# Kernel optimization log

Measured on AMD Instinct MI355X. Metric: run time of the kernel, lower is better.

## Reference

```python
import jax, jax.numpy as jnp
import numpy as np


def setup_inputs() -> dict:
    key = jax.random.key(0)
    ks = jax.random.split(key, 5)
    B, T, C, H, E = 8, 2048, 1024, 2048, 8
    n_layer = 12
    x = jax.random.normal(ks[0], (B, T, C), dtype=jnp.float32)
    w_router = jax.random.normal(ks[1], (C, E), dtype=jnp.float32) * 0.02
    w_c_fc = jax.random.normal(ks[2], (E, C, H), dtype=jnp.float32) * 0.02
    w_gate = jax.random.normal(ks[3], (E, C, H), dtype=jnp.float32) * 0.02
    w_c_proj = jax.random.normal(ks[4], (E, H, C), dtype=jnp.float32) * (0.02 * (2 * n_layer) ** -0.5)
    return {
        "x": x, "w_router": w_router, "w_c_fc": w_c_fc,
        "w_gate": w_gate, "w_c_proj": w_c_proj,
        "top_k": 2, "n_experts": E, "expert_capacity": 640,
    }


def reference(x, w_router, w_c_fc, w_gate, w_c_proj, top_k, n_experts, expert_capacity):
    B, T, C = x.shape
    # ---- router ----
    gate_logits = jnp.einsum('btc,ce->bte', x, w_router)
    gate_probs = jax.nn.softmax(gate_logits, axis=-1)  # (B,T,E)

    # ---- per-batch top-k dispatch (cumsum slot assignment + scatter) ----
    def dispatch(xb, pb):
        # xb: (T,C), pb: (T,E)
        topk_p, topk_i = jax.lax.top_k(pb, top_k)              # (T,k)
        ei = jnp.swapaxes(topk_i, 0, 1).ravel()                # (k*T,) k-major
        oh = jax.nn.one_hot(ei, n_experts, dtype=jnp.int32)    # (k*T,E)
        pos = jnp.cumsum(oh, axis=0) * oh - 1                  # slot within expert
        pos = jnp.swapaxes(pos.reshape(top_k, T, n_experts), 0, 1).max(axis=2)  # (T,k)
        ei = jnp.swapaxes(ei.reshape(top_k, T), 0, 1)          # (T,k)
        buf = jnp.zeros((n_experts, expert_capacity, C), dtype=xb.dtype)
        xr = jnp.repeat(xb, top_k, axis=0)                     # (T*k,C) token-major
        buf = buf.at[ei.ravel(), pos.ravel()].set(xr)          # overflow slots dropped
        return topk_p, pos, ei, buf

    topk_p, pos, ei, buf = jax.vmap(dispatch)(x, gate_probs)   # buf: (B,E,cap,C)

    # ---- batched expert SwiGLU GEMMs ----
    ein = jnp.swapaxes(buf, 0, 1).reshape(n_experts, B * expert_capacity, C)
    h = jnp.einsum('eti,eih->eth', ein, w_c_fc)
    g = jax.nn.silu(jnp.einsum('eti,eih->eth', ein, w_gate))
    o = jnp.einsum('eth,eho->eto', g * h, w_c_proj)
    eo = jnp.swapaxes(o.reshape(n_experts, B, expert_capacity, C), 0, 1)  # (B,E,cap,C)

    # ---- weighted combine gather ----
    def combine(eo_b, i_b, p_b, pr_b):
        sel = eo_b[i_b, p_b]                                   # (T,k,C)
        return jnp.sum(pr_b[..., None] * sel, axis=1)          # (T,C)

    y = jax.vmap(combine)(eo, ei, pos, topk_p)                 # (B,T,C)
    return y
```

## Files before the change

kernel.cpp:

```cpp
#include <hip/hip_runtime.h>
#include <stdint.h>

#define B_   8
#define T_   2048
#define C_   1024
#define H_   2048
#define E_   8
#define CAP_ 640
#define RPE_ (B_*CAP_)
#define BT_  (B_*T_)

typedef __attribute__((ext_vector_type(8))) short bf16x8;
typedef __attribute__((ext_vector_type(4))) float f32x4;

static __device__ __forceinline__ unsigned short f2bf(float f){
  union { float f; uint32_t u; } a; a.f = f;
  uint32_t u = a.u;
  uint32_t r = (u + 0x7FFFu + ((u >> 16) & 1u)) >> 16;
  return (unsigned short)r;
}

#define GLD16(gp, lp) __builtin_amdgcn_global_load_lds( \
    (__attribute__((address_space(1))) void*)(gp), \
    (__attribute__((address_space(3))) void*)(lp), 16, 0, 0)

#define VMW(N) asm volatile("s_waitcnt vmcnt(" #N ")" ::: "memory")
#define FENCE  asm volatile("" ::: "memory")
#define BARS   do { FENCE; __builtin_amdgcn_s_barrier(); __builtin_amdgcn_sched_barrier(0); } while(0)
#define BARE   do { __builtin_amdgcn_sched_barrier(0); FENCE; __builtin_amdgcn_s_barrier(); FENCE; } while(0)

#define LDA(H) do { \
  _Pragma("unroll") for (int ks_=0; ks_<2; ++ks_) \
  _Pragma("unroll") for (int f_=0; f_<4; ++f_) \
    pa[ks_][f_] = *(const bf16x8*)(bufc + (H)*16384u + aRow + (unsigned)f_*2048u + cc[ks_]); \
} while(0)
#define LDB(PB, H) do { \
  _Pragma("unroll") for (int ks_=0; ks_<2; ++ks_) \
  _Pragma("unroll") for (int n_=0; n_<2; ++n_) \
    PB[ks_][n_] = *(const bf16x8*)(bufc + 32768u + (H)*16384u + bRow + (unsigned)n_*2048u + cc[ks_]); \
} while(0)
#define MM16(Q, PB) do { \
  __builtin_amdgcn_s_setprio(1); \
  _Pragma("unroll") for (int ks_=0; ks_<2; ++ks_) \
  _Pragma("unroll") for (int f_=0; f_<4; ++f_) \
  _Pragma("unroll") for (int n_=0; n_<2; ++n_) \
    acc[Q][f_][n_] = __builtin_amdgcn_mfma_f32_16x16x32_bf16(pa[ks_][f_], PB[ks_][n_], acc[Q][f_][n_], 0,0,0); \
  __builtin_amdgcn_s_setprio(0); \
} while(0)

#define STG_A(H, T1) do { \
  unsigned kb_ = (unsigned)(T1)*128u; \
  unsigned db_ = ((unsigned)(T1)&1u)*65536u + (H)*16384u; \
  GLD16(pA##H##0 + kb_, lds + db_ + d0); \
  GLD16(pA##H##1 + kb_, lds + db_ + 8192u + d0); \
} while(0)
#define STG_B(H, T1) do { \
  unsigned kb_ = (unsigned)(T1)*128u; \
  unsigned db_ = ((unsigned)(T1)&1u)*65536u + 32768u + (H)*16384u; \
  GLD16(pB##H##0 + kb_, lds + db_ + d0); \
  GLD16(pB##H##1 + kb_, lds + db_ + 8192u + d0); \
} while(0)

__global__ __launch_bounds__(256) void router_kernel(
    const float* __restrict__ x, const float* __restrict__ wr,
    unsigned short* __restrict__ xbf, float* __restrict__ probs2, int* __restrict__ idx2)
{
  int bt = blockIdx.x;
  int tid = threadIdx.x;
  const float4 v = ((const float4*)(x + (size_t)bt*C_))[tid];
  ushort4 u;
  u.x = f2bf(v.x); u.y = f2bf(v.y); u.z = f2bf(v.z); u.w = f2bf(v.w);
  ((ushort4*)(xbf + (size_t)bt*C_))[tid] = u;

  double p[8];
  #pragma unroll
  for (int e=0;e<8;e++) p[e]=0.0;
  const float xv[4] = {v.x, v.y, v.z, v.w};
  #pragma unroll
  for (int j=0;j<4;j++){
    int c = tid*4+j;
    const float* wrow = wr + c*8;
    #pragma unroll
    for (int e=0;e<8;e++) p[e] += (double)xv[j] * (double)wrow[e];
  }
  __shared__ double red[8][256];
  #pragma unroll
  for (int e=0;e<8;e++) red[e][tid] = p[e];
  __syncthreads();
  for (int s=128; s>0; s>>=1){
    if (tid < s){
      #pragma unroll
      for (int e=0;e<8;e++) red[e][tid] += red[e][tid+s];
    }
    __syncthreads();
  }
  if (tid==0){
    double lg[8];
    #pragma unroll
    for (int e=0;e<8;e++) lg[e]=red[e][0];
    double mx = lg[0];
    #pragma unroll
    for (int e=1;e<8;e++) if (lg[e]>mx) mx=lg[e];
    double s=0.0, ex[8];
    #pragma unroll
    for (int e=0;e<8;e++){ ex[e]=exp(lg[e]-mx); s+=ex[e]; }
    int i1=0; double b1=ex[0];
    #pragma unroll
    for (int e=1;e<8;e++) if (ex[e]>b1){ b1=ex[e]; i1=e; }
    int i2=-1; double b2=-1.0;
    #pragma unroll
    for (int e=0;e<8;e++) if (e!=i1 && ex[e]>b2){ b2=ex[e]; i2=e; }
    probs2[bt*2+0] = (float)(b1/s);
    probs2[bt*2+1] = (float)(b2/s);
    idx2[bt*2+0] = i1;
    idx2[bt*2+1] = i2;
  }
}

__global__ __launch_bounds__(256) void transp_fcg_kernel(
    const float* __restrict__ fc, const float* __restrict__ gate,
    unsigned short* __restrict__ dst)
{
  __shared__ float t[32][33];
  int e = blockIdx.z;
  int n0 = blockIdx.x*32, k0 = blockIdx.y*32;
  int tx = threadIdx.x & 31, ty = threadIdx.x >> 5;
  #pragma unroll
  for (int sel=0; sel<2; ++sel){
    const float* s = (sel ? gate : fc) + ((size_t)e*C_ + k0)*H_ + n0;
    #pragma unroll
    for (int i=0;i<32;i+=8) t[ty+i][tx] = s[(size_t)(ty+i)*H_ + tx];
    __syncthreads();
    #pragma unroll
    for (int i=0;i<32;i+=8){
      int jj = ty+i;
      int drow = n0*2 + ((jj & 16) << 1) + sel*16 + (jj & 15);
      dst[((size_t)e*4096 + drow)*1024 + k0 + tx] = f2bf(t[tx][jj]);
    }
    __syncthreads();
  }
}

__global__ __launch_bounds__(256) void transp_kernel(
    const float* __restrict__ src, unsigned short* __restrict__ dst, int K, int N)
{
  __shared__ float t[32][33];
  int e = blockIdx.z;
  int n0 = blockIdx.x*32, k0 = blockIdx.y*32;
  int tx = threadIdx.x & 31, ty = threadIdx.x >> 5;
  const float* s = src + ((size_t)e*K + k0)*N + n0;
  #pragma unroll
  for (int i=0;i<32;i+=8) t[ty+i][tx] = s[(size_t)(ty+i)*N + tx];
  __syncthreads();
  unsigned short* d = dst + ((size_t)e*N + n0)*K + k0;
  #pragma unroll
  for (int i=0;i<32;i+=8) d[(size_t)(ty+i)*K + tx] = f2bf(t[tx][ty+i]);
}

__global__ void scan_kernel(const int* __restrict__ idx2, int* __restrict__ pos, int* __restrict__ cnt)
{
  int b = blockIdx.x, lane = threadIdx.x;
  unsigned long long below = (lane == 0) ? 0ull : (~0ull >> (64 - lane));
  int base = 0;
  for (int k=0;k<2;k++){
    for (int c0=0;c0<T_;c0+=64){
      int t = c0 + lane;
      int e = idx2[((b*T_ + t)<<1) + k];
      unsigned long long mym = 0; int addv = 0;
      #pragma unroll
      for (int ee=0; ee<8; ++ee){
        unsigned long long m = __ballot(e == ee);
        if (ee == e) mym = m;
        if (lane == ee) addv = __popcll(m);
      }
      int mybase = __shfl(base, e, 64);
      pos[((b*T_+t)<<1)+k] = mybase + __popcll(mym & below);
      base += addv;
    }
  }
  if (lane < 8) cnt[b*8 + lane] = (base < CAP_) ? base : CAP_;
}

__global__ void offsets_kernel(const int* __restrict__ cnt, int* __restrict__ off, int* __restrict__ Me)
{
  int e = threadIdx.x;
  if (e < 8){
    int s = 0;
    for (int b=0;b<8;b++){ off[e*8+b] = s; s += cnt[b*8+e]; }
    Me[e] = s;
  }
}

__global__ void fill_kernel(const int* __restrict__ idx2, const int* __restrict__ pos,
                            const int* __restrict__ off, const float* __restrict__ probs2,
                            int* __restrict__ token_src, float* __restrict__ row_prob)
{
  int a = blockIdx.x*256 + threadIdx.x;
  if (a >= BT_*2) return;
  int bt = a >> 1, k = a & 1;
  int b = bt >> 11;
  int e = idx2[bt*2+k];
  int p = pos[bt*2+k];
  if (p < CAP_){
    int r = e*RPE_ + off[e*8+b] + p;
    token_src[r] = bt;
    row_prob[r] = probs2[bt*2+k];
  }
}

__global__ __launch_bounds__(512, 2) void gemm1_kernel(
    const unsigned short* __restrict__ xbf,
    const unsigned short* __restrict__ wifcg,
    const int* __restrict__ token_src,
    const int* __restrict__ Me,
    unsigned short* __restrict__ act,
    int e0)
{
  const int lin = blockIdx.x;
  const int ez = lin / 320;
  const int r_ = lin % 320;
  const int xcd = r_ & 7, slot = r_ >> 3;
  const int nt = xcd + ((slot / 20) << 3);
  const int mt = slot % 20;
  const int e = e0 + ez;
  const int M = Me[e];
  if (mt*256 >= M) return;

  __shared__ __align__(16) unsigned char lds[131072];

  const int tid = threadIdx.x;
  const int w = tid >> 6, l = tid & 63;
  const int wm = w >> 2, wn = w & 3;
  const int l15 = l & 15, g0 = l >> 4;
  const unsigned d0 = (unsigned)tid * 16u;

  const int srow0 = tid >> 3, c0 = tid & 7;
  const unsigned scb = (unsigned)((c0 ^ (srow0 & 7)) * 16);
  const unsigned char* gA = (const unsigned char*)xbf;
  const unsigned char* gB = (const unsigned char*)wifcg;
  const int abase = e*RPE_ + mt*256;
  const unsigned char* pA00 = gA + (size_t)token_src[abase +       srow0]*2048u + scb;
  const unsigned char* pA01 = gA + (size_t)token_src[abase +  64 + srow0]*2048u + scb;
  const unsigned char* pA10 = gA + (size_t)token_src[abase + 128 + srow0]*2048u + scb;
  const unsigned char* pA11 = gA + (size_t)token_src[abase + 192 + srow0]*2048u + scb;
  const size_t bbase = (size_t)(ez*4096 + nt*256 + srow0);
  const unsigned char* pB00 = gB + (bbase +   0)*2048u + scb;
  const unsigned char* pB01 = gB + (bbase +  64)*2048u + scb;
  const unsigned char* pB10 = gB + (bbase + 128)*2048u + scb;
  const unsigned char* pB11 = gB + (bbase + 192)*2048u + scb;

  const unsigned aRow = (unsigned)((wm*64 + l15) * 128);
  const unsigned bRow = (unsigned)((wn*32 + l15) * 128);
  unsigned cc[2];
  cc[0] = (unsigned)(((0*4 + g0) ^ (l15 & 7)) * 16);
  cc[1] = (unsigned)(((1*4 + g0) ^ (l15 & 7)) * 16);

  f32x4 acc[4][4][2];
  #pragma unroll
  for (int p=0;p<4;++p)
    #pragma unroll
    for (int f=0;f<4;++f)
      #pragma unroll
      for (int n=0;n<2;++n) acc[p][f][n] = (f32x4){0.f,0.f,0.f,0.f};

  bf16x8 pa[2][4], pb0[2][2], pb1[2][2];

  STG_A(0,0); STG_B(0,0); STG_B(1,0); STG_A(1,0);
  VMW(4);
  FENCE; __builtin_amdgcn_s_barrier(); FENCE;

  const int NT = 16;
  for (int t = 0; t < NT-1; ++t){
    const unsigned char* bufc = lds + (unsigned)(t&1)*65536u;
    LDA(0); LDB(pb0,0); STG_A(0,t+1); VMW(4); BARS; MM16(0,pb0); BARE;
    LDB(pb1,1);         STG_B(0,t+1); VMW(4); BARS; MM16(1,pb1); BARE;
    LDA(1);             STG_B(1,t+1);         BARS; MM16(2,pb0); BARE;
                        STG_A(1,t+1); VMW(4); BARS; MM16(3,pb1); BARE;
  }
  {
    const unsigned char* bufc = lds + (unsigned)((NT-1)&1)*65536u;
    LDA(0); LDB(pb0,0); VMW(2); BARS; MM16(0,pb0); BARE;
    LDB(pb1,1);         VMW(0); BARS; MM16(1,pb1); BARE;
    LDA(1);                     BARS; MM16(2,pb0); BARE;
                                BARS; MM16(3,pb1); BARE;
  }

  const int r4 = (l >> 4) * 4;
  #pragma unroll
  for (int p=0;p<4;++p){
    const int ah = p>>1, bh = p&1;
    #pragma unroll
    for (int f=0;f<4;++f){
      const int grow = mt*256 + ah*128 + wm*64 + f*16 + r4;
      const int hcol = nt*128 + bh*64 + wn*16 + l15;
      #pragma unroll
      for (int r=0;r<4;++r){
        float h = acc[p][f][0][r];
        float gv = acc[p][f][1][r];
        float a = (gv / (1.f + __expf(-gv))) * h;
        act[((size_t)ez*RPE_ + grow + r)*(size_t)H_ + hcol] = f2bf(a);
      }
    }
  }
}

__global__ __launch_bounds__(512, 2) void gemm2_kernel(
    const unsigned short* __restrict__ act,
    const unsigned short* __restrict__ wprojT,
    const int* __restrict__ token_src,
    const float* __restrict__ row_prob,
    const int* __restrict__ Me,
    float* __restrict__ y,
    int e0)
{
  const int ez = blockIdx.z, e = e0 + ez, mt = blockIdx.y, nt = blockIdx.x;
  const int M = Me[e];
  if (mt*256 >= M) return;

  __shared__ __align__(16) unsigned char lds[131072];

  const int tid = threadIdx.x;
  const int w = tid >> 6, l = tid & 63;
  const int wm = w >> 2, wn = w & 3;
  const int l15 = l & 15, g0 = l >> 4;
  const unsigned d0 = (unsigned)tid * 16u;

  const int srow0 = tid >> 3, c0 = tid & 7;
  const unsigned scb = (unsigned)((c0 ^ (srow0 & 7)) * 16);
  const unsigned char* gA = (const unsigned char*)act;
  const unsigned char* gB = (const unsigned char*)wprojT;
  const size_t abase = (size_t)(ez*RPE_ + mt*256 + srow0);
  const unsigned char* pA00 = gA + (abase +   0)*4096u + scb;
  const unsigned char* pA01 = gA + (abase +  64)*4096u + scb;
  const unsigned char* pA10 = gA + (abase + 128)*4096u + scb;
  const unsigned char* pA11 = gA + (abase + 192)*4096u + scb;
  const size_t bbase = (size_t)(ez*C_ + nt*256 + srow0);
  const unsigned char* pB00 = gB + (bbase +   0)*4096u + scb;
  const unsigned char* pB01 = gB + (bbase +  64)*4096u + scb;
  const unsigned char* pB10 = gB + (bbase + 128)*4096u + scb;
  const unsigned char* pB11 = gB + (bbase + 192)*4096u + scb;

  const unsigned aRow = (unsigned)((wm*64 + l15) * 128);
  const unsigned bRow = (unsigned)((wn*32 + l15) * 128);
  unsigned cc[2];
  cc[0] = (unsigned)(((0*4 + g0) ^ (l15 & 7)) * 16);
  cc[1] = (unsigned)(((1*4 + g0) ^ (l15 & 7)) * 16);

  f32x4 acc[4][4][2];
  #pragma unroll
  for (int p=0;p<4;++p)
    #pragma unroll
    for (int f=0;f<4;++f)
      #pragma unroll
      for (int n=0;n<2;++n) acc[p][f][n] = (f32x4){0.f,0.f,0.f,0.f};

  bf16x8 pa[2][4], pb0[2][2], pb1[2][2];

  STG_A(0,0); STG_B(0,0); STG_B(1,0); STG_A(1,0);
  VMW(4);
  FENCE; __builtin_amdgcn_s_barrier(); FENCE;

  const int NT = 32;
  for (int t = 0; t < NT-1; ++t){
    const unsigned char* bufc = lds + (unsigned)(t&1)*65536u;
    LDA(0); LDB(pb0,0); STG_A(0,t+1); VMW(4); BARS; MM16(0,pb0); BARE;
    LDB(pb1,1);         STG_B(0,t+1); VMW(4); BARS; MM16(1,pb1); BARE;
    LDA(1);             STG_B(1,t+1);         BARS; MM16(2,pb0); BARE;
                        STG_A(1,t+1); VMW(4); BARS; MM16(3,pb1); BARE;
  }
  {
    const unsigned char* bufc = lds + (unsigned)((NT-1)&1)*65536u;
    LDA(0); LDB(pb0,0); VMW(2); BARS; MM16(0,pb0); BARE;
    LDB(pb1,1);         VMW(0); BARS; MM16(1,pb1); BARE;
    LDA(1);                     BARS; MM16(2,pb0); BARE;
                                BARS; MM16(3,pb1); BARE;
  }

  const int r4 = (l >> 4) * 4;
  #pragma unroll
  for (int p=0;p<4;++p){
    const int ah = p>>1, bh = p&1;
    #pragma unroll
    for (int f=0;f<4;++f){
      #pragma unroll
      for (int r=0;r<4;++r){
        const int rloc = mt*256 + ah*128 + wm*64 + f*16 + r4 + r;
        if (rloc < M){
          const int bt = token_src[e*RPE_ + rloc];
          const float pp = row_prob[e*RPE_ + rloc];
          float* yrow = y + (size_t)bt*C_;
          const int colb = nt*256 + bh*128 + wn*32 + l15;
          atomicAdd(yrow + colb,      pp * acc[p][f][0][r]);
          atomicAdd(yrow + colb + 16, pp * acc[p][f][1][r]);
        }
      }
    }
  }
}

extern "C" void kernel_launch(void* const* d_in, const int* in_sizes, int n_in,
                              void* d_out, int out_size, void* d_ws, size_t ws_size,
                              hipStream_t stream)
{
  const float* x   = (const float*)d_in[0];
  const float* wr  = (const float*)d_in[1];
  const float* wfc = (const float*)d_in[2];
  const float* wg  = (const float*)d_in[3];
  const float* wpj = (const float*)d_in[4];
  float* y = (float*)d_out;

  unsigned char* ws = (unsigned char*)d_ws;
  const size_t szXBF  = (size_t)BT_*C_*2;
  const size_t szFCGc = (size_t)2*4096*1024*2;
  const size_t szWPc  = (size_t)2*C_*H_*2;
  const size_t szFCGa = (size_t)E_*4096*1024*2;
  const size_t szWPa  = (size_t)E_*C_*H_*2;
  const size_t szMISC = 3*131072 + 2*(size_t)E_*RPE_*4 + 1024;

  const size_t need_small = szXBF + szFCGc + szWPc + (size_t)2*RPE_*H_*2 + szMISC;
  const size_t need_big2  = szXBF + szFCGa + szWPa  + (size_t)2*RPE_*H_*2 + szMISC;
  const size_t need_big4  = szXBF + szFCGa + szWPa  + (size_t)4*RPE_*H_*2 + szMISC;
  if (ws_size < need_small) return;
  const bool big4 = (ws_size >= need_big4);
  const bool big  = big4 || (ws_size >= need_big2);
  const int  ne   = big4 ? 4 : 2;

  const size_t szFCG = big ? szFCGa : szFCGc;
  const size_t szWP  = big ? szWPa  : szWPc;
  const size_t szACT = (size_t)ne*RPE_*H_*2;

  size_t oXBF = 0;
  size_t oFCG = oXBF + szXBF;
  size_t oWP  = oFCG + szFCG;
  size_t oACT = oWP  + szWP;
  size_t oM   = oACT + szACT;

  unsigned short* xbf    = (unsigned short*)(ws + oXBF);
  unsigned short* wifcg  = (unsigned short*)(ws + oFCG);
  unsigned short* wprojT = (unsigned short*)(ws + oWP);
  unsigned short* actc   = (unsigned short*)(ws + oACT);

  float* probs2    = (float*)(ws + oM);
  int*   idx2      = (int*)(ws + oM + 1*131072);
  int*   pos       = (int*)(ws + oM + 2*131072);
  int*   token_src = (int*)(ws + oM + 3*131072);
  float* row_prob  = (float*)(ws + oM + 3*131072 + (size_t)E_*RPE_*4);
  int*   cnt       = (int*)(ws + oM + 3*131072 + 2*(size_t)E_*RPE_*4);
  int*   off       = cnt + 64;
  int*   Me        = off + 64;

  hipMemsetAsync(y, 0, (size_t)out_size*4, stream);
  hipMemsetAsync(token_src, 0, (size_t)E_*RPE_*4, stream);

  router_kernel<<<BT_, 256, 0, stream>>>(x, wr, xbf, probs2, idx2);
  scan_kernel<<<B_, 64, 0, stream>>>(idx2, pos, cnt);
  offsets_kernel<<<1, 64, 0, stream>>>(cnt, off, Me);
  fill_kernel<<<(BT_*2+255)/256, 256, 0, stream>>>(idx2, pos, off, probs2, token_src, row_prob);

  if (big){
    transp_fcg_kernel<<<dim3(H_/32, C_/32, E_), 256, 0, stream>>>(wfc, wg, wifcg);
    transp_kernel<<<dim3(C_/32, H_/32, E_), 256, 0, stream>>>(wpj, wprojT, H_, C_);
  }

  for (int e0 = 0; e0 < E_; e0 += ne){
    unsigned short* wfcg_c = wifcg;
    unsigned short* wpj_c  = wprojT;
    if (big){
      wfcg_c = wifcg  + (size_t)e0*4096*1024;
      wpj_c  = wprojT + (size_t)e0*C_*H_;
    } else {
      transp_fcg_kernel<<<dim3(H_/32, C_/32, ne), 256, 0, stream>>>(
          wfc + (size_t)e0*C_*H_, wg + (size_t)e0*C_*H_, wifcg);
      transp_kernel<<<dim3(C_/32, H_/32, ne), 256, 0, stream>>>(
          wpj + (size_t)e0*H_*C_, wprojT, H_, C_);
    }
    gemm1_kernel<<<dim3(320*ne), 512, 0, stream>>>(
        xbf, wfcg_c, token_src, Me, actc, e0);
    gemm2_kernel<<<dim3(4, 20, ne), 512, 0, stream>>>(
        actc, wpj_c, token_src, row_prob, Me, y, e0);
  }
}
```

Measured before the change: 792.0 us.

## Rewrite gemm2 with 128x128 tiles, 256 threads, and XCD-aware block mapping

Replaces the 256x256-tile, 512-thread, hand-pipelined gemm2 with a simpler 128x128-tile kernel of 256 threads. It uses double-buffered 64 KB LDS and a flat 1D grid that maps blocks so neighbouring M tiles spread across XCDs. Smaller tiles raise occupancy and finer skipping of empty rows beyond Me. In exchange the kernel does more redundant global loads per FLOP and drops the interleaved fine-grained pipelining of the old schedule.

Result: faster. 741.3 us (-6.4%).

```diff
diff --git a/kernel.cpp b/kernel.cpp
--- a/kernel.cpp
+++ b/kernel.cpp
@@ -304,7 +304,7 @@
   }
 }
 
-__global__ __launch_bounds__(512, 2) void gemm2_kernel(
+__global__ __launch_bounds__(256) void gemm2_kernel(
     const unsigned short* __restrict__ act,
     const unsigned short* __restrict__ wprojT,
     const int* __restrict__ token_src,
@@ -313,85 +313,98 @@
     float* __restrict__ y,
     int e0)
 {
-  const int ez = blockIdx.z, e = e0 + ez, mt = blockIdx.y, nt = blockIdx.x;
+  const int lin = blockIdx.x;
+  const int ez = lin / 320;
+  const int r_ = lin % 320;
+  const int xcd = r_ & 7, slot = r_ >> 3;
+  const int mt = xcd + ((slot >> 3) << 3);
+  const int nt = slot & 7;
+  const int e = e0 + ez;
   const int M = Me[e];
-  if (mt*256 >= M) return;
-
-  __shared__ __align__(16) unsigned char lds[131072];
+  if (mt*128 >= M) return;
+
+  __shared__ __align__(16) unsigned char lds[2][32768];
 
   const int tid = threadIdx.x;
   const int w = tid >> 6, l = tid & 63;
-  const int wm = w >> 2, wn = w & 3;
-  const int l15 = l & 15, g0 = l >> 4;
-  const unsigned d0 = (unsigned)tid * 16u;
-
-  const int srow0 = tid >> 3, c0 = tid & 7;
-  const unsigned scb = (unsigned)((c0 ^ (srow0 & 7)) * 16);
+  const int wrow = w >> 1, wcol = w & 1;
+  const int r8 = l >> 3;
+  const unsigned swz16 = (unsigned)(((l & 7) ^ r8) * 16);
+
+  unsigned ldsOff[4];
+  size_t offA[4], offB[4];
+  #pragma unroll
+  for (int j = 0; j < 4; ++j){
+    int row = w*32 + j*8 + r8;
+    offA[j] = ((size_t)(ez*RPE_ + mt*128 + row))*4096u + swz16;
+    offB[j] = ((size_t)(ez*C_   + nt*128 + row))*4096u + swz16;
+    ldsOff[j] = (unsigned)(w*32 + j*8) * 128u;
+  }
+
+  f32x4 acc[4][4];
+  #pragma unroll
+  for (int i=0;i<4;i++)
+    #pragma unroll
+    for (int j=0;j<4;j++) acc[i][j] = (f32x4){0.f,0.f,0.f,0.f};
+
   const unsigned char* gA = (const unsigned char*)act;
   const unsigned char* gB = (const unsigned char*)wprojT;
-  const size_t abase = (size_t)(ez*RPE_ + mt*256 + srow0);
-  const unsigned char* pA00 = gA + (abase +   0)*4096u + scb;
-  const unsigned char* pA01 = gA + (abase +  64)*4096u + scb;
-  const unsigned char* pA10 = gA + (abase + 128)*4096u + scb;
-  const unsigned char* pA11 = gA + (abase + 192)*4096u + scb;
-  const size_t bbase = (size_t)(ez*C_ + nt*256 + srow0);
-  const unsigned char* pB00 = gB + (bbase +   0)*4096u + scb;
-  const unsigned char* pB01 = gB + (bbase +  64)*4096u + scb;
-  const unsigned char* pB10 = gB + (bbase + 128)*4096u + scb;
-  const unsigned char* pB11 = gB + (bbase + 192)*4096u + scb;
-
-  const unsigned aRow = (unsigned)((wm*64 + l15) * 128);
-  const unsigned bRow = (unsigned)((wn*32 + l15) * 128);
-  unsigned cc[2];
-  cc[0] = (unsigned)(((0*4 + g0) ^ (l15 & 7)) * 16);
-  cc[1] = (unsigned)(((1*4 + g0) ^ (l15 & 7)) * 16);
-
-  f32x4 acc[4][4][2];
-  #pragma unroll
-  for (int p=0;p<4;++p)
-    #pragma unroll
-    for (int f=0;f<4;++f)
-      #pragma unroll
-      for (int n=0;n<2;++n) acc[p][f][n] = (f32x4){0.f,0.f,0.f,0.f};
-
-  bf16x8 pa[2][4], pb0[2][2], pb1[2][2];
-
-  STG_A(0,0); STG_B(0,0); STG_B(1,0); STG_A(1,0);
-  VMW(4);
-  FENCE; __builtin_amdgcn_s_barrier(); FENCE;
-
+
+  auto stage = [&](int kt, int bb){
+    const unsigned kb = (unsigned)kt * 128u;
+    #pragma unroll
+    for (int j=0;j<4;++j) GLD16(gA + offA[j] + kb, &lds[bb][0]     + ldsOff[j]);
+    #pragma unroll
+    for (int j=0;j<4;++j) GLD16(gB + offB[j] + kb, &lds[bb][16384] + ldsOff[j]);
+  };
+  auto compute = [&](int bb){
+    #pragma unroll
+    for (int kh=0; kh<2; ++kh){
+      bf16x8 afr[4], bfr[4];
+      #pragma unroll
+      for (int fm=0; fm<4; ++fm){
+        int row = wrow*64 + fm*16 + (l & 15);
+        int gnum = kh*4 + (l >> 4);
+        int byt = row*128 + ((gnum ^ (row & 7)) * 16);
+        afr[fm] = *(const bf16x8*)(&lds[bb][0] + byt);
+      }
+      #pragma unroll
+      for (int fn=0; fn<4; ++fn){
+        int row = wcol*64 + fn*16 + (l & 15);
+        int gnum = kh*4 + (l >> 4);
+        int byt = row*128 + ((gnum ^ (row & 7)) * 16);
+        bfr[fn] = *(const bf16x8*)(&lds[bb][16384] + byt);
+      }
+      #pragma unroll
+      for (int fm=0; fm<4; ++fm)
+        #pragma unroll
+        for (int fn=0; fn<4; ++fn)
+          acc[fm][fn] = __builtin_amdgcn_mfma_f32_16x16x32_bf16(afr[fm], bfr[fn], acc[fm][fn], 0,0,0);
+    }
+  };
+
+  stage(0, 0);
+  __syncthreads();
   const int NT = 32;
-  for (int t = 0; t < NT-1; ++t){
-    const unsigned char* bufc = lds + (unsigned)(t&1)*65536u;
-    LDA(0); LDB(pb0,0); STG_A(0,t+1); VMW(4); BARS; MM16(0,pb0); BARE;
-    LDB(pb1,1);         STG_B(0,t+1); VMW(4); BARS; MM16(1,pb1); BARE;
-    LDA(1);             STG_B(1,t+1);         BARS; MM16(2,pb0); BARE;
-                        STG_A(1,t+1); VMW(4); BARS; MM16(3,pb1); BARE;
-  }
-  {
-    const unsigned char* bufc = lds + (unsigned)((NT-1)&1)*65536u;
-    LDA(0); LDB(pb0,0); VMW(2); BARS; MM16(0,pb0); BARE;
-    LDB(pb1,1);         VMW(0); BARS; MM16(1,pb1); BARE;
-    LDA(1);                     BARS; MM16(2,pb0); BARE;
-                                BARS; MM16(3,pb1); BARE;
-  }
-
-  const int r4 = (l >> 4) * 4;
-  #pragma unroll
-  for (int p=0;p<4;++p){
-    const int ah = p>>1, bh = p&1;
-    #pragma unroll
-    for (int f=0;f<4;++f){
-      #pragma unroll
-      for (int r=0;r<4;++r){
-        const int rloc = mt*256 + ah*128 + wm*64 + f*16 + r4 + r;
-        if (rloc < M){
-          const int bt = token_src[e*RPE_ + rloc];
-          const float pp = row_prob[e*RPE_ + rloc];
-          float* yrow = y + (size_t)bt*C_;
-          const int colb = nt*256 + bh*128 + wn*32 + l15;
-          atomicAdd(yrow + colb,      pp * acc[p][f][0][r]);
-          atomicAdd(yrow + colb + 16, pp * acc[p][f][1][r]);
+  for (int kt = 0; kt < NT; ++kt){
+    if (kt+1 < NT) stage(kt+1, (kt+1)&1);
+    compute(kt&1);
+    __syncthreads();
+  }
+
+  #pragma unroll
+  for (int fm=0; fm<4; ++fm){
+    #pragma unroll
+    for (int r=0; r<4; ++r){
+      int rloc = mt*128 + wrow*64 + fm*16 + (l>>4)*4 + r;
+      if (rloc < M){
+        int bt  = token_src[e*RPE_ + rloc];
+        float p = row_prob[e*RPE_ + rloc];
+        float* yrow = y + (size_t)bt*C_;
+        #pragma unroll
+        for (int fn=0; fn<4; ++fn){
+          int col = nt*128 + wcol*64 + fn*16 + (l & 15);
+          atomicAdd(yrow + col, p * acc[fm][fn][r]);
         }
       }
     }
@@ -476,7 +489,7 @@
     }
     gemm1_kernel<<<dim3(320*ne), 512, 0, stream>>>(
         xbf, wfcg_c, token_src, Me, actc, e0);
-    gemm2_kernel<<<dim3(4, 20, ne), 512, 0, stream>>>(
+    gemm2_kernel<<<dim3(320*ne), 256, 0, stream>>>(
         actc, wpj_c, token_src, row_prob, Me, y, e0);
   }
 }
```
